# Optimization experiments

Hardware: AMD Instinct MI355X
Metric: run time of the kernel (lower is better)

Reference implementation:

```python
import jax, jax.numpy as jnp
import numpy as np

# Routing structure from the torch module
GT0 = [[0,1,0,0,1,0],[0,1,0,0,0,1],[0,0,1,0,1,0],[0,0,1,0,0,1],[0,0,0,1,1,0],[0,0,0,1,0,1]]
NCLS = 6
K = 1  # top-k

def _expert_pairs():
    # For class i, expert index m = 1+(j-1)*5+(k-1) maps to atom1[j-1] -> atom2[k-1].
    pairs = []
    for i in range(NCLS):
        p = [(j - 1, k - 1) for j in range(1, 6) for k in range(1, 6)
             if j != k and GT0[i][j] == 1 and GT0[i][k] == 1]
        pairs.append(p)
    return pairs

PAIRS = _expert_pairs()  # each class has exactly 2 (atom1, atom2) pairs

B, P, D, H = 64, 256, 768, 3072

def setup_inputs() -> dict:
    key = jax.random.key(0)
    ks = jax.random.split(key, 8)
    s = 0.02
    x = jax.random.normal(ks[0], (B, NCLS + P, D), dtype=jnp.float32)
    mids = jax.random.randint(ks[1], (B,), 0, 6)
    moe0_W1 = jax.random.normal(ks[2], (D, H), dtype=jnp.float32) * s
    moe0_b1 = jnp.zeros((H,), jnp.float32)
    moe0_W2 = jax.random.normal(ks[3], (H, D), dtype=jnp.float32) * s
    moe0_b2 = jnp.zeros((D,), jnp.float32)
    A1_W = jax.random.normal(ks[4], (5, D, H), dtype=jnp.float32) * s  # atom1 linears
    A1_b = jnp.zeros((5, H), jnp.float32)
    A2_W = jax.random.normal(ks[5], (5, H, D), dtype=jnp.float32) * s  # atom2 linears
    A2_b = jnp.zeros((5, D), jnp.float32)
    G_W = jax.random.normal(ks[6], (NCLS, D, 2), dtype=jnp.float32) * s  # per-class gates (2 experts each, no bias)
    return {"x": x, "moe0_W1": moe0_W1, "moe0_b1": moe0_b1, "moe0_W2": moe0_W2,
            "moe0_b2": moe0_b2, "A1_W": A1_W, "A1_b": A1_b, "A2_W": A2_W,
            "A2_b": A2_b, "G_W": G_W, "mids": mids}

def _gelu(t):
    return jax.nn.gelu(t, approximate=False)  # torch nn.GELU default = erf

def reference(x, moe0_W1, moe0_b1, moe0_W2, moe0_b2, A1_W, A1_b, A2_W, A2_b, G_W, mids):
    cls_tokens = x[:, :NCLS]          # [B, 6, D]
    patch_tokens = x[:, NCLS:]        # [B, P, D]
    patch_out = _gelu(patch_tokens @ moe0_W1 + moe0_b1) @ moe0_W2 + moe0_b2  # [B, P, D]
    cls_outs = []
    for i in range(NCLS):
        tok = cls_tokens[:, i]        # [B, D]
        eouts = [ _gelu(tok @ A1_W[a] + A1_b[a]) @ A2_W[c] + A2_b[c] for (a, c) in PAIRS[i] ]
        out = jnp.stack(eouts, axis=-1)                 # [B, D, E=2]
        gate = jax.nn.softmax(tok @ G_W[i], axis=-1)    # [B, E]
        # top-k masking (k=1 < E=2): keep gates strictly above the (k+1)-th largest
        thr = jnp.sort(gate, axis=-1)[..., -(K + 1)]    # [B]
        mask = (gate > thr[..., None]).astype(gate.dtype)
        g = gate * mask
        g = g / jnp.clip(jnp.sum(g, axis=-1, keepdims=True), 1e-6)
        cls_outs.append(jnp.sum(out * g[:, None, :], axis=-1))  # [B, D]
    cls_out = jnp.stack(cls_outs, axis=1)               # [B, 6, D]
    return jnp.concatenate([cls_out, patch_out], axis=1)  # [B, 6+P, D]
```

## Files before the change

### kernel.cpp

```cpp
#include <hip/hip_runtime.h>
#include <hip/hip_bf16.h>

#define DD 768
#define HH 3072
#define BB 64
#define TT 262

typedef __bf16 bf16x8 __attribute__((ext_vector_type(8)));
typedef float f32x4 __attribute__((ext_vector_type(4)));
typedef unsigned short u16;
typedef unsigned int u32;

__device__ __constant__ int A_FIRST[12]  = {0,3, 0,4, 1,3, 1,4, 2,3, 2,4};
__device__ __constant__ int A_SECOND[12] = {3,0, 4,0, 3,1, 4,1, 3,2, 4,2};

__device__ __forceinline__ float gelu_f(float x) {
  float n2t = x * fmaf(x * x, -0.0713548163f, -1.5957691216f);
  return x * __builtin_amdgcn_rcpf(1.0f + __expf(n2t));
}

__device__ __forceinline__ u16 f2bf(float x) {
  u32 u = __builtin_bit_cast(u32, x);
  return (u16)((u + 0x7fffu + ((u >> 16) & 1u)) >> 16);
}

__device__ __forceinline__ void load_lds16(const void* g, void* l) {
  __builtin_amdgcn_global_load_lds(
      (const __attribute__((address_space(1))) void*)g,
      (__attribute__((address_space(3))) void*)l,
      16, 0, 0);
}

__global__ void cast_x_kernel(const float* __restrict__ in, __hip_bfloat16* __restrict__ out, int n4) {
  int i = blockIdx.x * blockDim.x + threadIdx.x;
  if (i < n4) {
    float4 v = ((const float4*)in)[i];
    u16* o = (u16*)out + (size_t)i * 4;
    union { u16 s[4]; uint2 d; } pk;
    pk.s[0] = f2bf(v.x); pk.s[1] = f2bf(v.y); pk.s[2] = f2bf(v.z); pk.s[3] = f2bf(v.w);
    *(uint2*)o = pk.d;
  }
}

__global__ void transpose_cast6(const float* __restrict__ w, const float* __restrict__ a,
                                __hip_bfloat16* __restrict__ wt, __hip_bfloat16* __restrict__ at,
                                int R, int C) {
  __shared__ __hip_bfloat16 tile[32][33];
  int z = blockIdx.z;
  const float* ip = z ? (a + (size_t)(z - 1) * R * C) : w;
  __hip_bfloat16* op = z ? (at + (size_t)(z - 1) * R * C) : wt;
  int c0 = blockIdx.x * 32, r0 = blockIdx.y * 32;
  int tx = threadIdx.x & 31;
  int ty = threadIdx.x >> 5;
#pragma unroll
  for (int s = 0; s < 4; ++s) {
    int rr = ty * 4 + s;
    tile[rr][tx] = __float2bfloat16(ip[(size_t)(r0 + rr) * C + c0 + tx]);
  }
  __syncthreads();
#pragma unroll
  for (int s = 0; s < 4; ++s) {
    int cc = ty * 4 + s;
    op[(size_t)(c0 + cc) * R + r0 + tx] = tile[tx][cc];
  }
}

__global__ void gate_kernel(const float* __restrict__ x, const float* __restrict__ GW, int* __restrict__ sel) {
  int b = blockIdx.x, i = blockIdx.y;
  int lane = threadIdx.x;
  const float* tok = x + (size_t)(b * TT + i) * DD;
  const float* g = GW + (size_t)i * DD * 2;
  float p0 = 0.f, p1 = 0.f;
  for (int k = lane; k < DD; k += 64) {
    float t = tok[k];
    p0 += t * g[k * 2 + 0];
    p1 += t * g[k * 2 + 1];
  }
#pragma unroll
  for (int o = 32; o; o >>= 1) { p0 += __shfl_xor(p0, o); p1 += __shfl_xor(p1, o); }
  if (lane == 0) sel[i * 64 + b] = (p0 > p1) ? 0 : ((p1 > p0) ? 1 : 2);
}

__global__ void finalize_cls(const float* __restrict__ part, const float* __restrict__ A2b,
                             const int* __restrict__ sel, float* __restrict__ out) {
  int t = blockIdx.x * blockDim.x + threadIdx.x;
  int d4 = t % 192;
  int b = (t / 192) & 63;
  int cls = t / (192 * 64);
  int s = sel[cls * 64 + b];
  float4 res = make_float4(0.f, 0.f, 0.f, 0.f);
  if (s != 2) {
    int combo = cls * 2 + s;
    const float4* bb = (const float4*)(A2b + (size_t)A_SECOND[combo] * DD);
    res = bb[d4];
#pragma unroll
    for (int z = 0; z < 4; ++z) {
      const float4* p = (const float4*)(part + (((size_t)z * 12 + combo) * 64 + b) * DD);
      float4 v = p[d4];
      res.x += v.x; res.y += v.y; res.z += v.z; res.w += v.w;
    }
  }
  ((float4*)out)[(size_t)(b * TT + cls) * 192 + d4] = res;
}

template <int BM, int BN, int MODE>
__global__ __launch_bounds__(256, 2)
void gemm_k(const __hip_bfloat16* __restrict__ A,
            const __hip_bfloat16* __restrict__ Bw,
            const float* __restrict__ bias,
            void* __restrict__ Out,
            const int* __restrict__ sel) {
  constexpr int KDIM = (MODE == 0 || MODE == 2) ? DD : HH;
  constexpr int KITERS = (MODE == 3) ? 12 : KDIM / 64;
  constexpr int WAVES_M = (BM == 128) ? 2 : 1;
  constexpr int WAVES_N = 4 / WAVES_M;
  constexpr int MT = BM / (16 * WAVES_M);
  constexpr int NT = BN / (16 * WAVES_N);
  constexpr int CHA = BM / 32;
  constexpr int CHB = BN / 32;

  __shared__ __align__(16) char smem[(BM + BN) * 128];
  char* As = smem;
  char* Bs = smem + BM * 128;

  const int tid = threadIdx.x;
  const int lane = tid & 63;
  const int wave = tid >> 6;
  const int q = lane >> 4;
  const int r = lane & 15;
  const int wave_m = wave / WAVES_N;
  const int wave_n = wave % WAVES_N;

  int m0 = 0, n0, combo = 0, cls_i = 0, zsp = 0;
  size_t k0b = 0;
  const __hip_bfloat16* Bp = Bw;
  const float* biasp = bias;
  if constexpr (MODE == 0) {
    int bx = blockIdx.x;
    m0 = (bx / 12) * BM;
    n0 = (bx % 12) * BN;
  } else if constexpr (MODE == 1) {
    int bx = blockIdx.x;
    m0 = (bx / 6) * BM;
    n0 = (bx % 6) * BN;
  } else {
    n0 = blockIdx.x * BN;
    combo = blockIdx.y;
    cls_i = combo >> 1;
    int e = (MODE == 2) ? A_FIRST[combo] : A_SECOND[combo];
    Bp = Bw + (size_t)e * DD * HH;
    if constexpr (MODE == 2) biasp = bias + e * HH;
    if constexpr (MODE == 3) { zsp = blockIdx.z; k0b = (size_t)zsp * 768 * 2; }
  }

  const int trow = tid >> 3;
  const int sw = ((tid & 7) ^ (trow & 7)) << 4;
  size_t a_row_off;
  if constexpr (MODE == 0) {
    int m = m0 + trow;
    a_row_off = (size_t)((m >> 8) * TT + 6 + (m & 255)) * DD * 2;
  } else if constexpr (MODE == 1) {
    a_row_off = (size_t)(m0 + trow) * HH * 2;
  } else if constexpr (MODE == 2) {
    a_row_off = (size_t)(trow * TT + cls_i) * DD * 2;
  } else {
    a_row_off = (size_t)(combo * 64 + trow) * HH * 2 + k0b;
  }
  const char* gA0 = (const char*)A + a_row_off + sw;
  const char* gB0 = (const char*)Bp + (size_t)(n0 + trow) * KDIM * 2 + k0b + sw;
  constexpr size_t ASTR = (size_t)32 * ((MODE == 0) ? DD : (MODE == 2) ? TT * DD : HH) * 2;
  constexpr size_t BSTR = (size_t)32 * KDIM * 2;
  const int wave_base = (tid & ~63) * 16;

  f32x4 acc[MT][NT];
#pragma unroll
  for (int i_ = 0; i_ < MT; ++i_)
#pragma unroll
    for (int j_ = 0; j_ < NT; ++j_) acc[i_][j_] = (f32x4){0.f, 0.f, 0.f, 0.f};

  const char* a_rd = As + (wave_m * (MT * 16) + r) * 128;
  const char* b_rd = Bs + (wave_n * (NT * 16) + r) * 128;
  const int sa = ((q ^ (r & 7)) << 4);

  for (int kt = 0; kt < KITERS; ++kt) {
#pragma unroll
    for (int u = 0; u < CHA; ++u) load_lds16(gA0 + u * ASTR, As + u * 4096 + wave_base);
#pragma unroll
    for (int u = 0; u < CHB; ++u) load_lds16(gB0 + u * BSTR, Bs + u * 4096 + wave_base);
    gA0 += 128;
    gB0 += 128;
    __syncthreads();
#pragma unroll
    for (int t = 0; t < 2; ++t) {
      const int so = sa ^ (t << 6);
      bf16x8 af[MT], bf[NT];
#pragma unroll
      for (int i_ = 0; i_ < MT; ++i_) af[i_] = *(const bf16x8*)(a_rd + i_ * 2048 + so);
#pragma unroll
      for (int j_ = 0; j_ < NT; ++j_) bf[j_] = *(const bf16x8*)(b_rd + j_ * 2048 + so);
#pragma unroll
      for (int i_ = 0; i_ < MT; ++i_)
#pragma unroll
        for (int j_ = 0; j_ < NT; ++j_)
          acc[i_][j_] = __builtin_amdgcn_mfma_f32_16x16x32_bf16(bf[j_], af[i_], acc[i_][j_], 0, 0, 0);
    }
    __syncthreads();
  }

#pragma unroll
  for (int i_ = 0; i_ < MT; ++i_) {
    int m_g = m0 + wave_m * (MT * 16) + i_ * 16 + r;
#pragma unroll
    for (int j_ = 0; j_ < NT; ++j_) {
      int nb = n0 + wave_n * (NT * 16) + j_ * 16 + q * 4;
      f32x4 v = acc[i_][j_];
      if constexpr (MODE != 3) {
        f32x4 bb = *(const f32x4*)(biasp + nb);
        v += bb;
      }
      if constexpr (MODE == 0) {
        union { u16 s[4]; uint2 d; } pk;
#pragma unroll
        for (int rg = 0; rg < 4; ++rg) pk.s[rg] = f2bf(gelu_f(v[rg]));
        *(uint2*)((u16*)Out + (size_t)m_g * HH + nb) = pk.d;
      } else if constexpr (MODE == 1) {
        int b = m_g >> 8, p = m_g & 255;
        *(f32x4*)((float*)Out + (size_t)(b * TT + 6 + p) * DD + nb) = v;
      } else if constexpr (MODE == 2) {
        union { u16 s[4]; uint2 d; } pk;
#pragma unroll
        for (int rg = 0; rg < 4; ++rg) pk.s[rg] = f2bf(gelu_f(v[rg]));
        *(uint2*)((u16*)Out + (size_t)(combo * 64 + m_g) * HH + nb) = pk.d;
      } else {
        *(f32x4*)((float*)Out + (((size_t)zsp * 12 + combo) * 64 + m_g) * DD + nb) = v;
      }
    }
  }
}

extern "C" void kernel_launch(void* const* d_in, const int* in_sizes, int n_in,
                              void* d_out, int out_size, void* d_ws, size_t ws_size,
                              hipStream_t stream) {
  const float* x   = (const float*)d_in[0];
  const float* W1  = (const float*)d_in[1];
  const float* b1  = (const float*)d_in[2];
  const float* W2  = (const float*)d_in[3];
  const float* b2  = (const float*)d_in[4];
  const float* A1W = (const float*)d_in[5];
  const float* A1b = (const float*)d_in[6];
  const float* A2W = (const float*)d_in[7];
  const float* A2b = (const float*)d_in[8];
  const float* GW  = (const float*)d_in[9];
  float* out = (float*)d_out;

  char* ws = (char*)d_ws;
  __hip_bfloat16* xb   = (__hip_bfloat16*)(ws + 0);
  __hip_bfloat16* W1t  = (__hip_bfloat16*)(ws + 25755648);
  __hip_bfloat16* W2t  = (__hip_bfloat16*)(ws + 30474240);
  __hip_bfloat16* A1t  = (__hip_bfloat16*)(ws + 35192832);
  __hip_bfloat16* A2t  = (__hip_bfloat16*)(ws + 58785792);
  __hip_bfloat16* hcls = (__hip_bfloat16*)(ws + 82378752);
  int* sel             = (int*)(ws + 87097344);
  __hip_bfloat16* hid  = (__hip_bfloat16*)(ws + 87099136);
  float* part          = (float*)(ws + 35192832);

  cast_x_kernel<<<12576, 256, 0, stream>>>(x, xb, 3219456);
  transpose_cast6<<<dim3(96, 24, 6), 256, 0, stream>>>(W1, A1W, W1t, A1t, DD, HH);
  transpose_cast6<<<dim3(24, 96, 6), 256, 0, stream>>>(W2, A2W, W2t, A2t, HH, DD);
  gate_kernel<<<dim3(64, 6), 64, 0, stream>>>(x, GW, sel);

  gemm_k<64, 128, 2><<<dim3(24, 12), 256, 0, stream>>>(xb, A1t, A1b, hcls, nullptr);
  gemm_k<64, 128, 3><<<dim3(6, 12, 4), 256, 0, stream>>>(hcls, A2t, nullptr, part, nullptr);
  finalize_cls<<<288, 256, 0, stream>>>(part, A2b, sel, out);

  gemm_k<128, 256, 0><<<1536, 256, 0, stream>>>(xb, W1t, b1, hid, nullptr);
  gemm_k<128, 128, 1><<<768, 256, 0, stream>>>(hid, W2t, b2, out, nullptr);
}
```

Baseline: 448.5 us.

## Merge preprocessing and expert GEMMs into fewer fused grid launches

Folds the x cast, the six weight transpose-casts and the gate computation into one preprocessing launch. The class-token expert GEMMs now share grids with the patch-token GEMMs (mega1, mega2), which cuts nine launches to three and lets the small expert work fill the tail waves of the large GEMMs. The second expert GEMM drops split-K and the finalize pass: it adds the bias and writes only the selected expert's output (or zeros) straight into out, using the gate selection. The patch GEMM blocks are also reordered into chunks of 16 M-tiles per N-tile, aiming for better L2 reuse. In exchange, the mega kernels reserve LDS for the larger tile shape, and the unsplit class GEMM gives each block a longer serial K loop.

```diff
diff --git a/kernel.cpp b/kernel.cpp
--- a/kernel.cpp
+++ b/kernel.cpp
@@ -31,87 +31,82 @@
       16, 0, 0);
 }
 
-__global__ void cast_x_kernel(const float* __restrict__ in, __hip_bfloat16* __restrict__ out, int n4) {
-  int i = blockIdx.x * blockDim.x + threadIdx.x;
-  if (i < n4) {
-    float4 v = ((const float4*)in)[i];
-    u16* o = (u16*)out + (size_t)i * 4;
+__global__ __launch_bounds__(256)
+void preproc(const float* __restrict__ x,
+             const float* __restrict__ W1, const float* __restrict__ A1W,
+             const float* __restrict__ W2, const float* __restrict__ A2W,
+             const float* __restrict__ GW,
+             __hip_bfloat16* __restrict__ xb,
+             __hip_bfloat16* __restrict__ W1t, __hip_bfloat16* __restrict__ A1t,
+             __hip_bfloat16* __restrict__ W2t, __hip_bfloat16* __restrict__ A2t,
+             int* __restrict__ sel) {
+  __shared__ __hip_bfloat16 tile[32][33];
+  const int bx = blockIdx.x;
+  const int tid = threadIdx.x;
+  if (bx < 12576) {
+    int i = bx * 256 + tid;
+    float4 v = ((const float4*)x)[i];
     union { u16 s[4]; uint2 d; } pk;
     pk.s[0] = f2bf(v.x); pk.s[1] = f2bf(v.y); pk.s[2] = f2bf(v.z); pk.s[3] = f2bf(v.w);
-    *(uint2*)o = pk.d;
-  }
-}
-
-__global__ void transpose_cast6(const float* __restrict__ w, const float* __restrict__ a,
-                                __hip_bfloat16* __restrict__ wt, __hip_bfloat16* __restrict__ at,
-                                int R, int C) {
-  __shared__ __hip_bfloat16 tile[32][33];
-  int z = blockIdx.z;
-  const float* ip = z ? (a + (size_t)(z - 1) * R * C) : w;
-  __hip_bfloat16* op = z ? (at + (size_t)(z - 1) * R * C) : wt;
-  int c0 = blockIdx.x * 32, r0 = blockIdx.y * 32;
-  int tx = threadIdx.x & 31;
-  int ty = threadIdx.x >> 5;
-#pragma unroll
-  for (int s = 0; s < 4; ++s) {
-    int rr = ty * 4 + s;
-    tile[rr][tx] = __float2bfloat16(ip[(size_t)(r0 + rr) * C + c0 + tx]);
-  }
-  __syncthreads();
-#pragma unroll
-  for (int s = 0; s < 4; ++s) {
-    int cc = ty * 4 + s;
-    op[(size_t)(c0 + cc) * R + r0 + tx] = tile[tx][cc];
-  }
-}
-
-__global__ void gate_kernel(const float* __restrict__ x, const float* __restrict__ GW, int* __restrict__ sel) {
-  int b = blockIdx.x, i = blockIdx.y;
-  int lane = threadIdx.x;
-  const float* tok = x + (size_t)(b * TT + i) * DD;
-  const float* g = GW + (size_t)i * DD * 2;
-  float p0 = 0.f, p1 = 0.f;
-  for (int k = lane; k < DD; k += 64) {
-    float t = tok[k];
-    p0 += t * g[k * 2 + 0];
-    p1 += t * g[k * 2 + 1];
-  }
-#pragma unroll
-  for (int o = 32; o; o >>= 1) { p0 += __shfl_xor(p0, o); p1 += __shfl_xor(p1, o); }
-  if (lane == 0) sel[i * 64 + b] = (p0 > p1) ? 0 : ((p1 > p0) ? 1 : 2);
-}
-
-__global__ void finalize_cls(const float* __restrict__ part, const float* __restrict__ A2b,
-                             const int* __restrict__ sel, float* __restrict__ out) {
-  int t = blockIdx.x * blockDim.x + threadIdx.x;
-  int d4 = t % 192;
-  int b = (t / 192) & 63;
-  int cls = t / (192 * 64);
-  int s = sel[cls * 64 + b];
-  float4 res = make_float4(0.f, 0.f, 0.f, 0.f);
-  if (s != 2) {
-    int combo = cls * 2 + s;
-    const float4* bb = (const float4*)(A2b + (size_t)A_SECOND[combo] * DD);
-    res = bb[d4];
-#pragma unroll
-    for (int z = 0; z < 4; ++z) {
-      const float4* p = (const float4*)(part + (((size_t)z * 12 + combo) * 64 + b) * DD);
-      float4 v = p[d4];
-      res.x += v.x; res.y += v.y; res.z += v.z; res.w += v.w;
-    }
-  }
-  ((float4*)out)[(size_t)(b * TT + cls) * 192 + d4] = res;
+    *(uint2*)((u16*)xb + (size_t)i * 4) = pk.d;
+  } else if (bx < 40224) {
+    int R, C;
+    const float* ip;
+    __hip_bfloat16* op;
+    int t;
+    if (bx < 26400) {
+      t = bx - 12576; R = DD; C = HH;
+      int z = t / 2304; t %= 2304;
+      ip = z ? (A1W + (size_t)(z - 1) * DD * HH) : W1;
+      op = z ? (A1t + (size_t)(z - 1) * DD * HH) : W1t;
+    } else {
+      t = bx - 26400; R = HH; C = DD;
+      int z = t / 2304; t %= 2304;
+      ip = z ? (A2W + (size_t)(z - 1) * DD * HH) : W2;
+      op = z ? (A2t + (size_t)(z - 1) * DD * HH) : W2t;
+    }
+    int ctiles = C >> 5;
+    int c0 = (t % ctiles) * 32, r0 = (t / ctiles) * 32;
+    int tx = tid & 31, ty = tid >> 5;
+#pragma unroll
+    for (int s = 0; s < 4; ++s) {
+      int rr = ty * 4 + s;
+      tile[rr][tx] = __float2bfloat16(ip[(size_t)(r0 + rr) * C + c0 + tx]);
+    }
+    __syncthreads();
+#pragma unroll
+    for (int s = 0; s < 4; ++s) {
+      int cc = ty * 4 + s;
+      op[(size_t)(c0 + cc) * R + r0 + tx] = tile[tx][cc];
+    }
+  } else {
+    int unit = (bx - 40224) * 4 + (tid >> 6);
+    int lane = tid & 63;
+    int b = unit & 63, i = unit >> 6;
+    const float* tok = x + (size_t)(b * TT + i) * DD;
+    const float* g = GW + (size_t)i * DD * 2;
+    float p0 = 0.f, p1 = 0.f;
+    for (int k = lane; k < DD; k += 64) {
+      float tv = tok[k];
+      p0 += tv * g[k * 2 + 0];
+      p1 += tv * g[k * 2 + 1];
+    }
+#pragma unroll
+    for (int o = 32; o; o >>= 1) { p0 += __shfl_xor(p0, o); p1 += __shfl_xor(p1, o); }
+    if (lane == 0) sel[i * 64 + b] = (p0 > p1) ? 0 : ((p1 > p0) ? 1 : 2);
+  }
 }
 
 template <int BM, int BN, int MODE>
-__global__ __launch_bounds__(256, 2)
-void gemm_k(const __hip_bfloat16* __restrict__ A,
-            const __hip_bfloat16* __restrict__ Bw,
-            const float* __restrict__ bias,
-            void* __restrict__ Out,
-            const int* __restrict__ sel) {
+__device__ __forceinline__
+void gemm_body(char* __restrict__ smem, int bx,
+               const __hip_bfloat16* __restrict__ A,
+               const __hip_bfloat16* __restrict__ Bw,
+               const float* __restrict__ bias,
+               void* __restrict__ Out,
+               const int* __restrict__ sel) {
   constexpr int KDIM = (MODE == 0 || MODE == 2) ? DD : HH;
-  constexpr int KITERS = (MODE == 3) ? 12 : KDIM / 64;
+  constexpr int KITERS = KDIM / 64;
   constexpr int WAVES_M = (BM == 128) ? 2 : 1;
   constexpr int WAVES_N = 4 / WAVES_M;
   constexpr int MT = BM / (16 * WAVES_M);
@@ -119,7 +114,6 @@
   constexpr int CHA = BM / 32;
   constexpr int CHB = BN / 32;
 
-  __shared__ __align__(16) char smem[(BM + BN) * 128];
   char* As = smem;
   char* Bs = smem + BM * 128;
 
@@ -131,26 +125,33 @@
   const int wave_m = wave / WAVES_N;
   const int wave_n = wave % WAVES_N;
 
-  int m0 = 0, n0, combo = 0, cls_i = 0, zsp = 0;
-  size_t k0b = 0;
+  int m0 = 0, n0, combo = 0, cls_i = 0;
   const __hip_bfloat16* Bp = Bw;
   const float* biasp = bias;
   if constexpr (MODE == 0) {
-    int bx = blockIdx.x;
-    m0 = (bx / 12) * BM;
-    n0 = (bx % 12) * BN;
+    int chunk = bx / 192, local = bx % 192;
+    int nb = local / 16, mloc = local % 16;
+    m0 = (chunk * 16 + mloc) * BM;
+    n0 = nb * BN;
   } else if constexpr (MODE == 1) {
-    int bx = blockIdx.x;
-    m0 = (bx / 6) * BM;
+    int chunk = bx / 96, local = bx % 96;
+    int nb = local / 16, mloc = local % 16;
+    m0 = (chunk * 16 + mloc) * BM;
+    n0 = nb * BN;
+  } else if constexpr (MODE == 2) {
+    n0 = (bx % 24) * BN;
+    combo = bx / 24;
+    cls_i = combo >> 1;
+    int e = A_FIRST[combo];
+    Bp = Bw + (size_t)e * DD * HH;
+    biasp = bias + e * HH;
+  } else {
     n0 = (bx % 6) * BN;
-  } else {
-    n0 = blockIdx.x * BN;
-    combo = blockIdx.y;
+    combo = bx / 6;
     cls_i = combo >> 1;
-    int e = (MODE == 2) ? A_FIRST[combo] : A_SECOND[combo];
+    int e = A_SECOND[combo];
     Bp = Bw + (size_t)e * DD * HH;
-    if constexpr (MODE == 2) biasp = bias + e * HH;
-    if constexpr (MODE == 3) { zsp = blockIdx.z; k0b = (size_t)zsp * 768 * 2; }
+    biasp = bias + e * DD;
   }
 
   const int trow = tid >> 3;
@@ -164,10 +165,10 @@
   } else if constexpr (MODE == 2) {
     a_row_off = (size_t)(trow * TT + cls_i) * DD * 2;
   } else {
-    a_row_off = (size_t)(combo * 64 + trow) * HH * 2 + k0b;
+    a_row_off = (size_t)(combo * 64 + trow) * HH * 2;
   }
   const char* gA0 = (const char*)A + a_row_off + sw;
-  const char* gB0 = (const char*)Bp + (size_t)(n0 + trow) * KDIM * 2 + k0b + sw;
+  const char* gB0 = (const char*)Bp + (size_t)(n0 + trow) * KDIM * 2 + sw;
   constexpr size_t ASTR = (size_t)32 * ((MODE == 0) ? DD : (MODE == 2) ? TT * DD : HH) * 2;
   constexpr size_t BSTR = (size_t)32 * KDIM * 2;
   const int wave_base = (tid & ~63) * 16;
@@ -214,10 +215,8 @@
     for (int j_ = 0; j_ < NT; ++j_) {
       int nb = n0 + wave_n * (NT * 16) + j_ * 16 + q * 4;
       f32x4 v = acc[i_][j_];
-      if constexpr (MODE != 3) {
-        f32x4 bb = *(const f32x4*)(biasp + nb);
-        v += bb;
-      }
+      f32x4 bb = *(const f32x4*)(biasp + nb);
+      v += bb;
       if constexpr (MODE == 0) {
         union { u16 s[4]; uint2 d; } pk;
 #pragma unroll
@@ -232,10 +231,39 @@
         for (int rg = 0; rg < 4; ++rg) pk.s[rg] = f2bf(gelu_f(v[rg]));
         *(uint2*)((u16*)Out + (size_t)(combo * 64 + m_g) * HH + nb) = pk.d;
       } else {
-        *(f32x4*)((float*)Out + (((size_t)zsp * 12 + combo) * 64 + m_g) * DD + nb) = v;
+        int s = sel[cls_i * 64 + m_g];
+        int j = combo & 1;
+        float* dst = (float*)Out + (size_t)(m_g * TT + cls_i) * DD + nb;
+        if (s == j) {
+          *(f32x4*)dst = v;
+        } else if (j == 0 && s == 2) {
+          *(f32x4*)dst = (f32x4){0.f, 0.f, 0.f, 0.f};
+        }
       }
     }
   }
+}
+
+__global__ __launch_bounds__(256, 2)
+void mega1(const __hip_bfloat16* __restrict__ xb, const __hip_bfloat16* __restrict__ W1t,
+           const float* __restrict__ b1, __hip_bfloat16* __restrict__ hid,
+           const __hip_bfloat16* __restrict__ A1t, const float* __restrict__ A1b,
+           __hip_bfloat16* __restrict__ hcls) {
+  __shared__ __align__(16) char smem[(128 + 256) * 128];
+  int bx = blockIdx.x;
+  if (bx < 1536) gemm_body<128, 256, 0>(smem, bx, xb, W1t, b1, hid, nullptr);
+  else           gemm_body<64, 128, 2>(smem, bx - 1536, xb, A1t, A1b, hcls, nullptr);
+}
+
+__global__ __launch_bounds__(256, 2)
+void mega2(const __hip_bfloat16* __restrict__ hid, const __hip_bfloat16* __restrict__ W2t,
+           const float* __restrict__ b2, float* __restrict__ out,
+           const __hip_bfloat16* __restrict__ hcls, const __hip_bfloat16* __restrict__ A2t,
+           const float* __restrict__ A2b, const int* __restrict__ sel) {
+  __shared__ __align__(16) char smem[(128 + 128) * 128];
+  int bx = blockIdx.x;
+  if (bx < 768) gemm_body<128, 128, 1>(smem, bx, hid, W2t, b2, out, nullptr);
+  else          gemm_body<64, 128, 3>(smem, bx - 768, hcls, A2t, A2b, out, sel);
 }
 
 extern "C" void kernel_launch(void* const* d_in, const int* in_sizes, int n_in,
@@ -262,17 +290,8 @@
   __hip_bfloat16* hcls = (__hip_bfloat16*)(ws + 82378752);
   int* sel             = (int*)(ws + 87097344);
   __hip_bfloat16* hid  = (__hip_bfloat16*)(ws + 87099136);
-  float* part          = (float*)(ws + 35192832);
-
-  cast_x_kernel<<<12576, 256, 0, stream>>>(x, xb, 3219456);
-  transpose_cast6<<<dim3(96, 24, 6), 256, 0, stream>>>(W1, A1W, W1t, A1t, DD, HH);
-  transpose_cast6<<<dim3(24, 96, 6), 256, 0, stream>>>(W2, A2W, W2t, A2t, HH, DD);
-  gate_kernel<<<dim3(64, 6), 64, 0, stream>>>(x, GW, sel);
-
-  gemm_k<64, 128, 2><<<dim3(24, 12), 256, 0, stream>>>(xb, A1t, A1b, hcls, nullptr);
-  gemm_k<64, 128, 3><<<dim3(6, 12, 4), 256, 0, stream>>>(hcls, A2t, nullptr, part, nullptr);
-  finalize_cls<<<288, 256, 0, stream>>>(part, A2b, sel, out);
-
-  gemm_k<128, 256, 0><<<1536, 256, 0, stream>>>(xb, W1t, b1, hid, nullptr);
-  gemm_k<128, 128, 1><<<768, 256, 0, stream>>>(hid, W2t, b2, out, nullptr);
-}
+
+  preproc<<<40320, 256, 0, stream>>>(x, W1, A1W, W2, A2W, GW, xb, W1t, A1t, W2t, A2t, sel);
+  mega1<<<1824, 256, 0, stream>>>(xb, W1t, b1, hid, A1t, A1b, hcls);
+  mega2<<<840, 256, 0, stream>>>(hid, W2t, b2, out, hcls, A2t, A2b, sel);
+}
```

New measurement: 392.0 us. -12.6%, faster.
